# Performance work log

Measured on AMD Instinct MI355X. Metric: run time of the kernel, lower is better.

## Reference

```python
import jax, jax.numpy as jnp
import numpy as np
from jax import lax

# ---- module hyperparameters (from init_kwargs) ----
B = 8          # number of point clouds in the batch
NP = 4096      # points per cloud
C_IN = 64      # input feature channels
RATIO = 0.25   # fps ratio -> M_PER = 1024 centroids per cloud
R = 0.2        # ball-query radius
K = 64         # max_num_neighbors (hardcoded in the torch forward)
BIG = 1e10     # sentinel distance for out-of-radius pairs


def _fps(p, m):
    """Farthest point sampling on one cloud p:[Np,3] -> m local indices.
    Deterministic start at index 0 (torch_geometric uses a random start)."""
    mind = jnp.sum((p - p[0]) ** 2, axis=-1)  # [Np] dist^2 to first pick

    def step(mind, _):
        nxt = jnp.argmax(mind)
        d = jnp.sum((p - p[nxt]) ** 2, axis=-1)
        return jnp.minimum(mind, d), nxt

    _, rest = lax.scan(step, mind, None, length=m - 1)
    return jnp.concatenate([jnp.zeros((1,), rest.dtype), rest])  # [m]


def _ball_knn(p, s):
    """Radius query with neighbor cap: for each sampled point, the K nearest
    points within radius R (same cloud). p:[Np,3], s:[m] -> idx [m,K], mask [m,K].
    Note: every centroid contains itself (d=0), so each row has >=1 valid entry."""
    q = p[s]                                              # [m,3]
    d2 = jnp.sum((q[:, None, :] - p[None, :, :]) ** 2, axis=-1)  # [m,Np]
    dm = jnp.where(d2 <= R * R, d2, BIG)
    negv, idx = lax.top_k(-dm, K)                         # nearest-K within ball
    return idx, (-negv) < (BIG * 0.5)


def setup_inputs() -> dict:
    key = jax.random.key(0)
    k = jax.random.split(key, 6)
    x = jax.random.normal(k[0], (B * NP, C_IN), dtype=jnp.float32)
    pos = jax.random.uniform(k[1], (B * NP, 3), dtype=jnp.float32)  # unit cube
    batch = jnp.repeat(jnp.arange(B, dtype=jnp.int32), NP)

    def lin(kk, fi, fo):
        return jax.random.normal(kk, (fi, fo), dtype=jnp.float32) / np.float32(np.sqrt(fi))

    W1 = lin(k[2], C_IN + 3, 64); b1 = jnp.zeros((64,), jnp.float32)
    W2 = lin(k[3], 64, 64);       b2 = jnp.zeros((64,), jnp.float32)
    W3 = lin(k[4], 64, 128);      b3 = jnp.zeros((128,), jnp.float32)
    return dict(x=x, pos=pos, batch=batch, W1=W1, b1=b1, W2=W2, b2=b2,
                W3=W3, b3=b3, num_graphs=B)


def reference(x, pos, batch, W1, b1, W2, b2, W3, b3, num_graphs):
    Bn = int(num_graphs)
    N = pos.shape[0]
    Np = N // Bn
    m = int(Np * RATIO)

    posb = pos.reshape(Bn, Np, 3)
    sel = jax.vmap(lambda p: _fps(p, m))(posb)          # [B,m] local idx
    nbr, mask = jax.vmap(_ball_knn)(posb, sel)          # [B,m,K]

    offs = jnp.arange(Bn, dtype=sel.dtype) * Np
    sel_g = (sel + offs[:, None]).reshape(-1)           # [M] global centroid idx
    nbr_g = (nbr + offs[:, None, None]).reshape(Bn * m, K)
    maskf = mask.reshape(Bn * m, K)

    pos_s = pos[sel_g]                                  # [M,3]
    rel = pos[nbr_g] - pos_s[:, None, :]                # [M,K,3] pos_j - pos_i
    h = jnp.concatenate([x[nbr_g], rel], axis=-1)       # [M,K,C_IN+3]
    # PointNetConv local_nn (Linear-ReLU-Linear-ReLU-Linear), max aggregation
    h = jax.nn.relu(h @ W1 + b1)
    h = jax.nn.relu(h @ W2 + b2)
    h = h @ W3 + b3                                     # [M,K,128]
    h = jnp.where(maskf[:, :, None], h, jnp.float32(-1e30))
    x_out = jnp.max(h, axis=1)                          # [M,128]

    return x_out, pos_s, batch[sel_g]
```

## Files before the change

### kernel.cpp

```cpp
#include <hip/hip_runtime.h>
#include <math.h>

#define NB   8
#define NPTS 4096
#define MPER 1024
#define MTOT (NB*MPER)
#define CIN  64
#define KNN  64
#define PUB  32
#define R2D  0.04000000000000001

typedef unsigned int u32;
typedef unsigned long long u64;
typedef float v2f __attribute__((ext_vector_type(2)));
using s16x8 = __attribute__((ext_vector_type(8))) short;
using f32x4 = __attribute__((ext_vector_type(4))) float;

__device__ __forceinline__ float d2f(float ax, float ay, float az,
                                     float bx, float by, float bz) {
    float dx = __fsub_rn(ax, bx);
    float dy = __fsub_rn(ay, by);
    float dz = __fsub_rn(az, bz);
    return __fadd_rn(__fadd_rn(__fmul_rn(dx, dx), __fmul_rn(dy, dy)),
                     __fmul_rn(dz, dz));
}

__device__ __forceinline__ v2f pk_add(v2f a, v2f b) {
    v2f d;
    asm("v_pk_add_f32 %0, %1, %2" : "=v"(d) : "v"(a), "v"(b));
    return d;
}
__device__ __forceinline__ v2f pk_mul(v2f a, v2f b) {
    v2f d;
    asm("v_pk_mul_f32 %0, %1, %2" : "=v"(d) : "v"(a), "v"(b));
    return d;
}

__device__ __forceinline__ unsigned short f2bf(float f) {
    u32 x = __float_as_uint(f);
    u32 r = (x + 0x7fffu + ((x >> 16) & 1u)) >> 16;
    return (unsigned short)r;
}
__device__ __forceinline__ u32 pk2(float a, float b) {
    return (u32)f2bf(a) | ((u32)f2bf(b) << 16);
}

__device__ __forceinline__ f32x4 mfma16(s16x8 a, s16x8 b, f32x4 c) {
    return __builtin_amdgcn_mfma_f32_16x16x32_bf16(a, b, c, 0, 0, 0);
}

__device__ __forceinline__ u64 wave_max_u64_dpp(u64 key)
{
#define DPPMAX(ctrl, rmask) do {                                                   \
        u32 lo_ = (u32)key;                                                        \
        u32 hi_ = (u32)(key >> 32);                                                \
        u32 plo = (u32)__builtin_amdgcn_update_dpp(                                \
            0, (int)lo_, ctrl, rmask, 0xf, false);                                 \
        u32 phi = (u32)__builtin_amdgcn_update_dpp(                                \
            0, (int)hi_, ctrl, rmask, 0xf, false);                                 \
        u64 pk = ((u64)phi << 32) | plo;                                           \
        if (pk > key) key = pk;                                                    \
    } while (0)
    DPPMAX(0x111, 0xf);
    DPPMAX(0x112, 0xf);
    DPPMAX(0x114, 0xf);
    DPPMAX(0x118, 0xf);
    DPPMAX(0x142, 0xa);
    DPPMAX(0x143, 0xc);
#undef DPPMAX
    return key;
}

#define W1T_U 6656
#define W2T_U 4608
#define W3T_U 9216
#define WTOT_U 20480

__global__ __launch_bounds__(256) void prep_weights(
    const float* __restrict__ W1, const float* __restrict__ W2,
    const float* __restrict__ W3, unsigned short* __restrict__ wsW,
    int* __restrict__ prog, int* __restrict__ wq)
{
    if (blockIdx.x == 80) {
        int t = threadIdx.x;
        if (t < NB) prog[t * 16] = -1;
        if (t == NB) *wq = 0;
        return;
    }
    int i = blockIdx.x * 256 + threadIdx.x;
    float v;
    if (i < W1T_U) {
        int cr = i / 104, k = i - cr * 104;
        v = (k < 67) ? W1[k * 64 + cr] : 0.0f;
    } else if (i < W1T_U + W2T_U) {
        int j = i - W1T_U;
        int cr = j / 72, k = j - cr * 72;
        v = (k < 64) ? W2[k * 64 + cr] : 0.0f;
    } else {
        int j = i - (W1T_U + W2T_U);
        int cr = j / 72, k = j - cr * 72;
        v = (k < 64) ? W3[k * 128 + cr] : 0.0f;
    }
    wsW[i] = f2bf(v);
}


__device__ __forceinline__ void fps_body(char* smem, const float* __restrict__ pos,
                                         int* __restrict__ sel, int* __restrict__ prog)
{
    const int b    = blockIdx.x;
    const int t    = threadIdx.x;
    const int lane = t & 63;
    const int wv   = t >> 6;
    const float* pb = pos + (size_t)b * NPTS * 3;

    float4* lp = (float4*)smem;
    u64*    part = (u64*)(smem + 65536);

    v2f px[8], py[8], pz[8], mind[8];
#pragma unroll
    for (int pr = 0; pr < 8; ++pr) {
        int j0 = (2 * pr + 0) * 256 + t;
        int j1 = (2 * pr + 1) * 256 + t;
        float x0 = pb[j0 * 3 + 0], y0 = pb[j0 * 3 + 1], z0 = pb[j0 * 3 + 2];
        float x1 = pb[j1 * 3 + 0], y1 = pb[j1 * 3 + 1], z1 = pb[j1 * 3 + 2];
        px[pr] = v2f{x0, x1}; py[pr] = v2f{y0, y1}; pz[pr] = v2f{z0, z1};
        mind[pr] = v2f{3.0e38f, 3.0e38f};
        lp[j0] = float4{x0, y0, z0, 0.f};
        lp[j1] = float4{x1, y1, z1, 0.f};
    }
    if (t == 0)
        __hip_atomic_store(&sel[b * MPER + 0], b * NPTS + 0,
                           __ATOMIC_RELAXED, __HIP_MEMORY_SCOPE_AGENT);
    __syncthreads();

    float4 c0 = lp[0];
    float cx = c0.x, cy = c0.y, cz = c0.z;

    for (int it = 1; it < MPER; ++it) {
        const v2f ncx = v2f{-cx, -cx};
        const v2f ncy = v2f{-cy, -cy};
        const v2f ncz = v2f{-cz, -cz};

        float bv = -1.0f; int bi = 0;
#pragma unroll
        for (int pr = 0; pr < 8; ++pr) {
            v2f dx = pk_add(px[pr], ncx);
            v2f dy = pk_add(py[pr], ncy);
            v2f dz = pk_add(pz[pr], ncz);
            v2f s  = pk_add(pk_mul(dx, dx), pk_mul(dy, dy));
            v2f d2 = pk_add(s, pk_mul(dz, dz));
            float m0 = fminf(mind[pr].x, d2.x);
            float m1 = fminf(mind[pr].y, d2.y);
            mind[pr].x = m0; mind[pr].y = m1;
            if (m0 > bv) { bv = m0; bi = (2 * pr + 0) * 256 + t; }
            if (m1 > bv) { bv = m1; bi = (2 * pr + 1) * 256 + t; }
        }

        u64 key = ((u64)__float_as_uint(bv) << 32) | (u32)(~bi);
        key = wave_max_u64_dpp(key);

        const int p = it & 1;
        if (lane == 63) part[p * 4 + wv] = key;
        __syncthreads();

        u64 k0 = part[p * 4 + 0];
        u64 k1 = part[p * 4 + 1];
        u64 k2 = part[p * 4 + 2];
        u64 k3 = part[p * 4 + 3];
        u64 ka = k0 > k1 ? k0 : k1;
        u64 kb = k2 > k3 ? k2 : k3;
        u64 km = ka > kb ? ka : kb;
        int pick = (int)(~(u32)km);

        float4 cc = lp[pick];
        cx = cc.x; cy = cc.y; cz = cc.z;
        if (t == 0) {
            __hip_atomic_store(&sel[b * MPER + it], b * NPTS + pick,
                               __ATOMIC_RELAXED, __HIP_MEMORY_SCOPE_AGENT);
            if ((it & (PUB - 1)) == (PUB - 1)) {
                asm volatile("s_waitcnt vmcnt(0)" ::: "memory");
                __hip_atomic_store(&prog[b * 16], it,
                                   __ATOMIC_RELAXED, __HIP_MEMORY_SCOPE_AGENT);
            }
        }
    }
}

__device__ __forceinline__ void worker_loop(
    char* smem, const float* __restrict__ pos, const float* __restrict__ x,
    const unsigned short* __restrict__ wsW,
    const float* __restrict__ b1, const float* __restrict__ b2,
    const float* __restrict__ b3,
    int* __restrict__ sel, int* __restrict__ prog, int* __restrict__ wq,
    float* __restrict__ out_x, float* __restrict__ out_pos,
    float* __restrict__ out_batch)
{
    const int t = threadIdx.x;
    const int l = t & 63, w = t >> 6, lr = l & 15, kg = l >> 4;

    unsigned short* sW   = (unsigned short*)smem;
    unsigned short* sA1  = (unsigned short*)(smem + 40960);
    unsigned short* sH1  = (unsigned short*)(smem + 54272);
    unsigned short* sH2  = (unsigned short*)(smem + 63488);
    float* cd   = (float*)(smem + 72704);
    int*   ci   = (int*)(smem + 74752);
    int*   nbrl = (int*)(smem + 76800);
    int*   scnt = (int*)(smem + 77056);
    float* sq   = (float*)(smem + 77072);
    int*   sslot= (int*)(smem + 77084);

    {
        const uint4* src = (const uint4*)wsW;
        uint4* dst = (uint4*)sW;
#pragma unroll
        for (int i = 0; i < 10; ++i) dst[t + 256 * i] = src[t + 256 * i];
    }
    float bias1[4], bias2[4];
#pragma unroll
    for (int nt = 0; nt < 4; ++nt) {
        bias1[nt] = b1[nt * 16 + lr];
        bias2[nt] = b2[nt * 16 + lr];
    }
    const float b3r = (t < 128) ? b3[t] : 0.0f;

    const unsigned short* W1t = sW;
    const unsigned short* W2t = sW + W1T_U;
    const unsigned short* W3t = sW + W1T_U + W2T_U;

    for (;;) {
        if (t == 0) {
            int s = __hip_atomic_fetch_add(wq, 1, __ATOMIC_RELAXED,
                                           __HIP_MEMORY_SCOPE_AGENT);
            sslot[0] = s;
            if (s < MTOT) {
                const int it = s >> 3, b = s & 7;
                const int c = b * MPER + it;
                int p_;
                do {
                    p_ = __hip_atomic_load(&prog[b * 16], __ATOMIC_RELAXED,
                                           __HIP_MEMORY_SCOPE_AGENT);
                    if (p_ < it) __builtin_amdgcn_s_sleep(32);
                } while (p_ < it);
                int sg = __hip_atomic_load(&sel[c], __ATOMIC_RELAXED,
                                           __HIP_MEMORY_SCOPE_AGENT);
                float qx = pos[(size_t)sg * 3 + 0];
                float qy = pos[(size_t)sg * 3 + 1];
                float qz = pos[(size_t)sg * 3 + 2];
                sq[0] = qx; sq[1] = qy; sq[2] = qz;
                out_pos[(size_t)c * 3 + 0] = qx;
                out_pos[(size_t)c * 3 + 1] = qy;
                out_pos[(size_t)c * 3 + 2] = qz;
                out_batch[c] = (float)b;
            }
        }
        __syncthreads();
        const int s = sslot[0];
        if (s >= MTOT) break;
        const int it = s >> 3, b = s & 7;
        const int c = b * MPER + it;
        const float qx = sq[0], qy = sq[1], qz = sq[2];

        const float* pb2 = pos + (size_t)b * NPTS * 3;
        int nw = 0;
        for (int r0 = 0; r0 < 1024; r0 += 64) {
            int j = w * 1024 + r0 + l;
            float xx = pb2[j * 3 + 0], yy = pb2[j * 3 + 1], zz = pb2[j * 3 + 2];
            float d2 = d2f(xx, yy, zz, qx, qy, qz);
            bool inside = ((double)d2 <= R2D);
            u64 m = __ballot(inside);
            if (inside) {
                int off = nw + __popcll(m & ((1ull << l) - 1ull));
                if (off < 128) { cd[w * 128 + off] = d2; ci[w * 128 + off] = j; }
            }
            nw += __popcll(m);
        }
        nw = min(nw, 128);
        if (l == 0) scnt[w] = nw;
        __syncthreads();
        const int n0 = scnt[0], n1 = scnt[1], n2 = scnt[2], n3 = scnt[3];
        const int ntot = n0 + n1 + n2 + n3;
        const int cnt = min(ntot, KNN);

        for (int f = t; f < ntot; f += 256) {
            int w2, i2;
            if (f < n0)                { w2 = 0; i2 = f; }
            else if (f < n0 + n1)      { w2 = 1; i2 = f - n0; }
            else if (f < n0 + n1 + n2) { w2 = 2; i2 = f - n0 - n1; }
            else                       { w2 = 3; i2 = f - n0 - n1 - n2; }
            float d = cd[w2 * 128 + i2]; int id = ci[w2 * 128 + i2];
            int rank = 0;
#pragma unroll
            for (int w3 = 0; w3 < 4; ++w3) {
                int nn = scnt[w3];
                for (int j = 0; j < nn; ++j) {
                    float dj = cd[w3 * 128 + j]; int ij = ci[w3 * 128 + j];
                    rank += (dj < d || (dj == d && ij < id)) ? 1 : 0;
                }
            }
            if (rank < KNN) nbrl[rank] = id;
        }
        __syncthreads();

        {
            const int k = t >> 2, g = t & 3;
            const bool valid = k < cnt;
            const int nbg = valid ? (b * NPTS + nbrl[k]) : 0;
            const float* xr = x + (size_t)nbg * CIN + g * 16;
            float4 f0, f1, f2, f3;
            if (valid) {
                f0 = *(const float4*)(xr + 0);
                f1 = *(const float4*)(xr + 4);
                f2 = *(const float4*)(xr + 8);
                f3 = *(const float4*)(xr + 12);
            } else {
                f0 = float4{0.f, 0.f, 0.f, 0.f};
                f1 = f0; f2 = f0; f3 = f0;
            }
            uint4 ua = { pk2(f0.x, f0.y), pk2(f0.z, f0.w), pk2(f1.x, f1.y), pk2(f1.z, f1.w) };
            uint4 ub = { pk2(f2.x, f2.y), pk2(f2.z, f2.w), pk2(f3.x, f3.y), pk2(f3.z, f3.w) };
            *(uint4*)&sA1[k * 104 + g * 16 + 0] = ua;
            *(uint4*)&sA1[k * 104 + g * 16 + 8] = ub;
            if (g == 0) {
                float r0 = 0.f, r1 = 0.f, r2 = 0.f;
                if (valid) {
                    r0 = __fsub_rn(pos[(size_t)nbg * 3 + 0], qx);
                    r1 = __fsub_rn(pos[(size_t)nbg * 3 + 1], qy);
                    r2 = __fsub_rn(pos[(size_t)nbg * 3 + 2], qz);
                }
                uint4 uz = { 0u, 0u, 0u, 0u };
                uint4 ur = { pk2(r0, r1), (u32)f2bf(r2), 0u, 0u };
                *(uint4*)&sA1[k * 104 + 64] = ur;
                *(uint4*)&sA1[k * 104 + 72] = uz;
                *(uint4*)&sA1[k * 104 + 80] = uz;
                *(uint4*)&sA1[k * 104 + 88] = uz;
                *(uint4*)&sA1[k * 104 + 96] = uz;
            }
        }
        __syncthreads();

        f32x4 acc1[4];
#pragma unroll
        for (int nt = 0; nt < 4; ++nt) acc1[nt] = f32x4{0.f, 0.f, 0.f, 0.f};
        {
            const int ao = (w * 16 + lr) * 104 + kg * 8;
            const int bo = lr * 104 + kg * 8;
#pragma unroll
            for (int kc = 0; kc < 3; ++kc) {
                s16x8 af = *(const s16x8*)&sA1[ao + kc * 32];
#pragma unroll
                for (int nt = 0; nt < 4; ++nt) {
                    s16x8 bf = *(const s16x8*)&W1t[bo + nt * 1664 + kc * 32];
                    acc1[nt] = mfma16(af, bf, acc1[nt]);
                }
            }
        }
#pragma unroll
        for (int nt = 0; nt < 4; ++nt) {
            const int col = nt * 16 + lr;
#pragma unroll
            for (int r = 0; r < 4; ++r) {
                const int row = w * 16 + kg * 4 + r;
                float v = fmaxf(acc1[nt][r] + bias1[nt], 0.0f);
                sH1[row * 72 + col] = f2bf(v);
            }
        }
        __syncthreads();

        f32x4 acc2[4];
#pragma unroll
        for (int nt = 0; nt < 4; ++nt) acc2[nt] = f32x4{0.f, 0.f, 0.f, 0.f};
        {
            const int ao = (w * 16 + lr) * 72 + kg * 8;
            const int bo = lr * 72 + kg * 8;
#pragma unroll
            for (int kc = 0; kc < 2; ++kc) {
                s16x8 af = *(const s16x8*)&sH1[ao + kc * 32];
#pragma unroll
                for (int nt = 0; nt < 4; ++nt) {
                    s16x8 bf = *(const s16x8*)&W2t[bo + nt * 1152 + kc * 32];
                    acc2[nt] = mfma16(af, bf, acc2[nt]);
                }
            }
        }
#pragma unroll
        for (int nt = 0; nt < 4; ++nt) {
            const int col = nt * 16 + lr;
#pragma unroll
            for (int r = 0; r < 4; ++r) {
                const int row = w * 16 + kg * 4 + r;
                float v = fmaxf(acc2[nt][r] + bias2[nt], 0.0f);
                sH2[row * 72 + col] = f2bf(v);
            }
        }
        __syncthreads();

        f32x4 acc3[8];
#pragma unroll
        for (int nt = 0; nt < 8; ++nt) acc3[nt] = f32x4{0.f, 0.f, 0.f, 0.f};
        {
            const int ao = (w * 16 + lr) * 72 + kg * 8;
            const int bo = lr * 72 + kg * 8;
#pragma unroll
            for (int kc = 0; kc < 2; ++kc) {
                s16x8 af = *(const s16x8*)&sH2[ao + kc * 32];
#pragma unroll
                for (int nt = 0; nt < 8; ++nt) {
                    s16x8 bf = *(const s16x8*)&W3t[bo + nt * 1152 + kc * 32];
                    acc3[nt] = mfma16(af, bf, acc3[nt]);
                }
            }
        }

        float pm[8];
#pragma unroll
        for (int nt = 0; nt < 8; ++nt) pm[nt] = -1e30f;
#pragma unroll
        for (int r = 0; r < 4; ++r) {
            const int row = w * 16 + kg * 4 + r;
            if (row < cnt) {
#pragma unroll
                for (int nt = 0; nt < 8; ++nt) pm[nt] = fmaxf(pm[nt], acc3[nt][r]);
            }
        }
#pragma unroll
        for (int nt = 0; nt < 8; ++nt) {
            pm[nt] = fmaxf(pm[nt], __shfl_xor(pm[nt], 16));
            pm[nt] = fmaxf(pm[nt], __shfl_xor(pm[nt], 32));
        }
        __syncthreads();
        float* pbuf = cd;
        if (kg == 0) {
#pragma unroll
            for (int nt = 0; nt < 8; ++nt) pbuf[w * 128 + nt * 16 + lr] = pm[nt];
        }
        __syncthreads();
        if (t < 128) {
            float m = fmaxf(fmaxf(pbuf[t], pbuf[128 + t]),
                            fmaxf(pbuf[256 + t], pbuf[384 + t]));
            out_x[(size_t)c * 128 + t] = m + b3r;
        }
    }
}

__global__ __launch_bounds__(256) void fused_kernel(
    const float* __restrict__ pos, const float* __restrict__ x,
    const unsigned short* __restrict__ wsW,
    const float* __restrict__ b1, const float* __restrict__ b2,
    const float* __restrict__ b3,
    int* __restrict__ sel, int* __restrict__ prog, int* __restrict__ wq,
    float* __restrict__ out_x, float* __restrict__ out_pos,
    float* __restrict__ out_batch)
{
    extern __shared__ char smem[];
    if (blockIdx.x < NB) {
        fps_body(smem, pos, sel, prog);
        __syncthreads();
    }
    worker_loop(smem, pos, x, wsW, b1, b2, b3, sel, prog, wq,
                out_x, out_pos, out_batch);
}

extern "C" void kernel_launch(void* const* d_in, const int* in_sizes, int n_in,
                              void* d_out, int out_size, void* d_ws, size_t ws_size,
                              hipStream_t stream)
{
    const float* x   = (const float*)d_in[0];
    const float* pos = (const float*)d_in[1];
    const float* W1 = (const float*)d_in[3];
    const float* b1 = (const float*)d_in[4];
    const float* W2 = (const float*)d_in[5];
    const float* b2 = (const float*)d_in[6];
    const float* W3 = (const float*)d_in[7];
    const float* b3 = (const float*)d_in[8];

    float* out_x     = (float*)d_out;
    float* out_pos   = out_x + (size_t)MTOT * 128;
    float* out_batch = out_pos + (size_t)MTOT * 3;

    int* sel  = (int*)d_ws;
    int* prog = sel + MTOT;
    int* wq   = prog + 128;
    unsigned short* wsW = (unsigned short*)(wq + 16);

    (void)hipFuncSetAttribute((const void*)fused_kernel,
                              hipFuncAttributeMaxDynamicSharedMemorySize, 86016);

    prep_weights<<<81, 256, 0, stream>>>(W1, W2, W3, wsW, prog, wq);
    fused_kernel<<<256, 256, 86016, stream>>>(pos, x, wsW, b1, b2, b3,
                                              sel, prog, wq,
                                              out_x, out_pos, out_batch);
}
```

Measured before the change: 703.9 us.

## Replace FPS progress counter with per-entry sentinel flags in sel array

The FPS producer no longer publishes a progress counter every 32 iterations. The sel array is pre-filled with -1, and FPS lanes 0-7 write selected indices in batches of 8. Workers spin directly on their own sel entry until it becomes non-negative. This is meant to cut the latency between a centroid being chosen and a worker starting on it, and to remove the waitcnt fence from the FPS critical path. The trade-off is more polling traffic on individual sel entries and no explicit ordering fence.

```diff
diff --git a/kernel.cpp b/kernel.cpp
--- a/kernel.cpp
+++ b/kernel.cpp
@@ -7,7 +7,6 @@
 #define MTOT (NB*MPER)
 #define CIN  64
 #define KNN  64
-#define PUB  32
 #define R2D  0.04000000000000001
 
 typedef unsigned int u32;
@@ -79,15 +78,19 @@
 __global__ __launch_bounds__(256) void prep_weights(
     const float* __restrict__ W1, const float* __restrict__ W2,
     const float* __restrict__ W3, unsigned short* __restrict__ wsW,
-    int* __restrict__ prog, int* __restrict__ wq)
-{
-    if (blockIdx.x == 80) {
-        int t = threadIdx.x;
-        if (t < NB) prog[t * 16] = -1;
-        if (t == NB) *wq = 0;
+    int* __restrict__ sel, int* __restrict__ wq)
+{
+    const int bid = blockIdx.x;
+    const int t = threadIdx.x;
+    if (bid >= 112) {
+        if (t == 0) *wq = 0;
         return;
     }
-    int i = blockIdx.x * 256 + threadIdx.x;
+    if (bid >= 80) {
+        sel[(bid - 80) * 256 + t] = -1;
+        return;
+    }
+    int i = bid * 256 + t;
     float v;
     if (i < W1T_U) {
         int cr = i / 104, k = i - cr * 104;
@@ -106,7 +109,7 @@
 
 
 __device__ __forceinline__ void fps_body(char* smem, const float* __restrict__ pos,
-                                         int* __restrict__ sel, int* __restrict__ prog)
+                                         int* __restrict__ sel)
 {
     const int b    = blockIdx.x;
     const int t    = threadIdx.x;
@@ -129,13 +132,11 @@
         lp[j0] = float4{x0, y0, z0, 0.f};
         lp[j1] = float4{x1, y1, z1, 0.f};
     }
-    if (t == 0)
-        __hip_atomic_store(&sel[b * MPER + 0], b * NPTS + 0,
-                           __ATOMIC_RELAXED, __HIP_MEMORY_SCOPE_AGENT);
     __syncthreads();
 
     float4 c0 = lp[0];
     float cx = c0.x, cy = c0.y, cz = c0.z;
+    int mypick = 0;
 
     for (int it = 1; it < MPER; ++it) {
         const v2f ncx = v2f{-cx, -cx};
@@ -175,14 +176,13 @@
 
         float4 cc = lp[pick];
         cx = cc.x; cy = cc.y; cz = cc.z;
-        if (t == 0) {
-            __hip_atomic_store(&sel[b * MPER + it], b * NPTS + pick,
-                               __ATOMIC_RELAXED, __HIP_MEMORY_SCOPE_AGENT);
-            if ((it & (PUB - 1)) == (PUB - 1)) {
-                asm volatile("s_waitcnt vmcnt(0)" ::: "memory");
-                __hip_atomic_store(&prog[b * 16], it,
+
+        if (t < 8) {
+            if ((it & 7) == t) mypick = pick;
+            if ((it & 7) == 7)
+                __hip_atomic_store(&sel[b * MPER + (it - 7) + t],
+                                   b * NPTS + mypick,
                                    __ATOMIC_RELAXED, __HIP_MEMORY_SCOPE_AGENT);
-            }
         }
     }
 }
@@ -192,7 +192,7 @@
     const unsigned short* __restrict__ wsW,
     const float* __restrict__ b1, const float* __restrict__ b2,
     const float* __restrict__ b3,
-    int* __restrict__ sel, int* __restrict__ prog, int* __restrict__ wq,
+    int* __restrict__ sel, int* __restrict__ wq,
     float* __restrict__ out_x, float* __restrict__ out_pos,
     float* __restrict__ out_batch)
 {
@@ -236,14 +236,12 @@
             if (s < MTOT) {
                 const int it = s >> 3, b = s & 7;
                 const int c = b * MPER + it;
-                int p_;
+                int sg;
                 do {
-                    p_ = __hip_atomic_load(&prog[b * 16], __ATOMIC_RELAXED,
+                    sg = __hip_atomic_load(&sel[c], __ATOMIC_RELAXED,
                                            __HIP_MEMORY_SCOPE_AGENT);
-                    if (p_ < it) __builtin_amdgcn_s_sleep(32);
-                } while (p_ < it);
-                int sg = __hip_atomic_load(&sel[c], __ATOMIC_RELAXED,
-                                           __HIP_MEMORY_SCOPE_AGENT);
+                    if (sg < 0) __builtin_amdgcn_s_sleep(64);
+                } while (sg < 0);
                 float qx = pos[(size_t)sg * 3 + 0];
                 float qy = pos[(size_t)sg * 3 + 1];
                 float qz = pos[(size_t)sg * 3 + 2];
@@ -448,16 +446,16 @@
     const unsigned short* __restrict__ wsW,
     const float* __restrict__ b1, const float* __restrict__ b2,
     const float* __restrict__ b3,
-    int* __restrict__ sel, int* __restrict__ prog, int* __restrict__ wq,
+    int* __restrict__ sel, int* __restrict__ wq,
     float* __restrict__ out_x, float* __restrict__ out_pos,
     float* __restrict__ out_batch)
 {
     extern __shared__ char smem[];
     if (blockIdx.x < NB) {
-        fps_body(smem, pos, sel, prog);
-        __syncthreads();
-    }
-    worker_loop(smem, pos, x, wsW, b1, b2, b3, sel, prog, wq,
+        fps_body(smem, pos, sel);
+        __syncthreads();
+    }
+    worker_loop(smem, pos, x, wsW, b1, b2, b3, sel, wq,
                 out_x, out_pos, out_batch);
 }
 
@@ -478,16 +476,15 @@
     float* out_pos   = out_x + (size_t)MTOT * 128;
     float* out_batch = out_pos + (size_t)MTOT * 3;
 
-    int* sel  = (int*)d_ws;
-    int* prog = sel + MTOT;
-    int* wq   = prog + 128;
+    int* sel = (int*)d_ws;
+    int* wq  = sel + MTOT;
     unsigned short* wsW = (unsigned short*)(wq + 16);
 
     (void)hipFuncSetAttribute((const void*)fused_kernel,
                               hipFuncAttributeMaxDynamicSharedMemorySize, 86016);
 
-    prep_weights<<<81, 256, 0, stream>>>(W1, W2, W3, wsW, prog, wq);
+    prep_weights<<<113, 256, 0, stream>>>(W1, W2, W3, wsW, sel, wq);
     fused_kernel<<<256, 256, 86016, stream>>>(pos, x, wsW, b1, b2, b3,
-                                              sel, prog, wq,
+                                              sel, wq,
                                               out_x, out_pos, out_batch);
 }
```

After: 677.8 us. 3.7% less time.
